# Optimization experiments

Measured on AMD Instinct MI355X. Metric: run time of the kernel, lower is better.

Reference implementation:

```python
import jax, jax.numpy as jnp
import numpy as np

N_NODES = 100000


def _sage_conv(x, edge_index, W_l, W_r, b):
    # PyG SAGEConv (mean aggr): out_i = lin_l(mean_{j in N(i)} x_j) + lin_r(x_i)
    src, dst = edge_index[0], edge_index[1]
    msg = x[src]  # [E, d] gather
    agg_sum = jax.ops.segment_sum(msg, dst, num_segments=N_NODES)  # [N, d]
    deg = jax.ops.segment_sum(jnp.ones((src.shape[0],), x.dtype), dst, num_segments=N_NODES)
    agg = agg_sum / jnp.maximum(deg, 1.0)[:, None]  # mean aggregation
    return agg @ W_l.T + b + x @ W_r.T


def setup_inputs() -> dict:
    key = jax.random.key(0)
    k = jax.random.split(key, 8)
    d_in, hidden, out = 64, 128, 128
    x = jax.random.normal(k[0], (N_NODES, d_in), dtype=jnp.float32)
    edge_index = jax.random.randint(k[1], (2, 1600000), 0, N_NODES, dtype=jnp.int64)
    s1 = 1.0 / np.sqrt(d_in)
    s2 = 1.0 / np.sqrt(hidden)
    return {
        "x": x,
        "edge_index": edge_index,
        "W1_l": jax.random.uniform(k[2], (hidden, d_in), jnp.float32, -s1, s1),
        "W1_r": jax.random.uniform(k[3], (hidden, d_in), jnp.float32, -s1, s1),
        "b1": jnp.zeros((hidden,), jnp.float32),
        "W2_l": jax.random.uniform(k[4], (out, hidden), jnp.float32, -s2, s2),
        "W2_r": jax.random.uniform(k[5], (out, hidden), jnp.float32, -s2, s2),
        "b2": jnp.zeros((out,), jnp.float32),
    }


def reference(x, edge_index, W1_l, W1_r, b1, W2_l, W2_r, b2):
    h = jax.nn.relu(_sage_conv(x, edge_index, W1_l, W1_r, b1))
    return _sage_conv(h, edge_index, W2_l, W2_r, b2)
```

## Files before the change

### kernel.cpp

```cpp
#include <hip/hip_runtime.h>

#define NN 100000
#define NE 1600000
#define SCAN_BLK 2048

#define BSH 9
#define NBUCK2 ((NN + 511) / 512)
#define CHUNK 8192
#define NCHK ((NE + CHUNK - 1) / CHUNK)
#define L2T (NBUCK2 * NCHK)
#define NSTRIP (NN / 32)

using bf16x8 = __attribute__((ext_vector_type(8))) short;
using f32x16 = __attribute__((ext_vector_type(16))) float;

__device__ __forceinline__ unsigned short f2bf(float f) {
    unsigned u = __float_as_uint(f);
    u += 0x7FFFu + ((u >> 16) & 1u);
    return (unsigned short)(u >> 16);
}
__device__ __forceinline__ float bf2f(unsigned short h) {
    return __uint_as_float(((unsigned)h) << 16);
}

__global__ __launch_bounds__(256) void hist2_kernel(const int* __restrict__ dst,
                                                    int* __restrict__ histm) {
    __shared__ int lh[256];
    int blk = blockIdx.x, tid = threadIdx.x;
    lh[tid] = 0;
    __syncthreads();
    int base = blk * CHUNK;
#pragma unroll
    for (int t = 0; t < CHUNK / 256; t++) {
        int e = base + t * 256 + tid;
        if (e < NE) atomicAdd(&lh[dst[e] >> BSH], 1);
    }
    __syncthreads();
    if (tid < NBUCK2) histm[tid * NCHK + blk] = lh[tid];
}

__global__ __launch_bounds__(256) void scan1_kernel(int* __restrict__ data,
                                                    int* __restrict__ bsums, int L) {
    __shared__ int s[256];
    int bid = blockIdx.x, tid = threadIdx.x;
    int base = bid * SCAN_BLK + tid * 8;
    int v[8];
    int sum = 0;
#pragma unroll
    for (int t = 0; t < 8; t++) {
        int idx = base + t;
        v[t] = (idx < L) ? data[idx] : 0;
        sum += v[t];
    }
    s[tid] = sum;
    __syncthreads();
    for (int off = 1; off < 256; off <<= 1) {
        int val = (tid >= off) ? s[tid - off] : 0;
        __syncthreads();
        s[tid] += val;
        __syncthreads();
    }
    int excl = s[tid] - sum;
    if (tid == 255) bsums[bid] = s[255];
    int run = excl;
#pragma unroll
    for (int t = 0; t < 8; t++) {
        int idx = base + t;
        if (idx < L) data[idx] = run;
        run += v[t];
    }
}

__global__ __launch_bounds__(64) void scan2_kernel(int* __restrict__ bsums, int n) {
    int tid = threadIdx.x;
    int orig = (tid < n) ? bsums[tid] : 0;
    int v = orig;
    for (int off = 1; off < 64; off <<= 1) {
        int nb = __shfl_up(v, off, 64);
        if (tid >= off) v += nb;
    }
    if (tid < n) bsums[tid] = v - orig;
}

__global__ __launch_bounds__(256) void scan_add_kernel(int* __restrict__ data,
                                                       const int* __restrict__ bsums, int L) {
    int i = blockIdx.x * 256 + threadIdx.x;
    if (i < L) data[i] += bsums[i / SCAN_BLK];
}

__global__ __launch_bounds__(256) void scatter2_kernel(const int* __restrict__ src,
                                                       const int* __restrict__ dst,
                                                       const int* __restrict__ histm,
                                                       int* __restrict__ tmp) {
    __shared__ int lcur[256];
    int blk = blockIdx.x, tid = threadIdx.x;
    if (tid < NBUCK2) lcur[tid] = histm[tid * NCHK + blk];
    __syncthreads();
    int base = blk * CHUNK;
#pragma unroll
    for (int t = 0; t < CHUNK / 256; t++) {
        int e = base + t * 256 + tid;
        if (e < NE) {
            int d = dst[e];
            int p = atomicAdd(&lcur[d >> BSH], 1);
            tmp[p] = src[e] | ((d & 511) << 17);
        }
    }
}

__global__ __launch_bounds__(256) void count_place_kernel(const int* __restrict__ histm,
                                                          const int* __restrict__ tmp,
                                                          int* __restrict__ rowptr,
                                                          int* __restrict__ esrc) {
    __shared__ int cnt[512];
    __shared__ int s[256];
    int b = blockIdx.x, tid = threadIdx.x;
    int beg = histm[b * NCHK];
    int end = (b == NBUCK2 - 1) ? NE : histm[(b + 1) * NCHK];

    cnt[tid] = 0; cnt[tid + 256] = 0;
    __syncthreads();
    for (int e = beg + tid; e < end; e += 256)
        atomicAdd(&cnt[tmp[e] >> 17], 1);
    __syncthreads();

    int c0 = cnt[2 * tid], c1 = cnt[2 * tid + 1];
    int sum = c0 + c1;
    s[tid] = sum;
    __syncthreads();
    for (int off = 1; off < 256; off <<= 1) {
        int val = (tid >= off) ? s[tid - off] : 0;
        __syncthreads();
        s[tid] += val;
        __syncthreads();
    }
    int o0 = beg + s[tid] - sum;
    int o1 = o0 + c0;
    cnt[2 * tid] = o0;
    cnt[2 * tid + 1] = o1;
    int node0 = (b << BSH) + 2 * tid;
    if (node0 < NN)     rowptr[node0]     = o0;
    if (node0 + 1 < NN) rowptr[node0 + 1] = o1;
    if (b == 0 && tid == 0) rowptr[NN] = NE;
    __syncthreads();

    for (int e = beg + tid; e < end; e += 256) {
        int v = tmp[e];
        int p = atomicAdd(&cnt[v >> 17], 1);
        esrc[p] = v & 0x1FFFF;
    }
}

__global__ __launch_bounds__(256) void cvt_kernel(const float* __restrict__ in,
                                                  unsigned short* __restrict__ out, int n4) {
    int i = blockIdx.x * 256 + threadIdx.x;
    if (i < n4) {
        float4 f = ((const float4*)in)[i];
        ((ushort4*)out)[i] = make_ushort4(f2bf(f.x), f2bf(f.y), f2bf(f.z), f2bf(f.w));
    }
}

__global__ __launch_bounds__(256) void agg64_kernel(const unsigned short* __restrict__ feat,
                                                    const int* __restrict__ rowptr,
                                                    const int* __restrict__ esrc,
                                                    unsigned short* __restrict__ agg) {
    int node = blockIdx.x * 4 + (threadIdx.x >> 6);
    int lane = threadIdx.x & 63;
    int es = lane >> 3;
    int fi = lane & 7;
    int beg = rowptr[node], end = rowptr[node + 1];

    float ax[8];
#pragma unroll
    for (int i = 0; i < 8; i++) ax[i] = 0.0f;

    int e = beg;
    for (; e + 15 < end; e += 16) {
        int sA = esrc[e + es];
        int sB = esrc[e + 8 + es];
        bf16x8 uA = *(const bf16x8*)(feat + (size_t)sA * 64 + fi * 8);
        bf16x8 uB = *(const bf16x8*)(feat + (size_t)sB * 64 + fi * 8);
#pragma unroll
        for (int i = 0; i < 8; i++)
            ax[i] += bf2f((unsigned short)uA[i]) + bf2f((unsigned short)uB[i]);
    }
    if (e + 7 < end) {
        int s = esrc[e + es];
        bf16x8 u = *(const bf16x8*)(feat + (size_t)s * 64 + fi * 8);
#pragma unroll
        for (int i = 0; i < 8; i++) ax[i] += bf2f((unsigned short)u[i]);
        e += 8;
    }
    if (es < end - e) {
        int s = esrc[e + es];
        bf16x8 u = *(const bf16x8*)(feat + (size_t)s * 64 + fi * 8);
#pragma unroll
        for (int i = 0; i < 8; i++) ax[i] += bf2f((unsigned short)u[i]);
    }

#pragma unroll
    for (int i = 0; i < 8; i++) {
        ax[i] += __shfl_xor(ax[i], 8);
        ax[i] += __shfl_xor(ax[i], 16);
        ax[i] += __shfl_xor(ax[i], 32);
    }
    if (es == 0) {
        float inv = 1.0f / fmaxf((float)(end - beg), 1.0f);
        bf16x8 o;
#pragma unroll
        for (int i = 0; i < 8; i++) o[i] = (short)f2bf(ax[i] * inv);
        *(bf16x8*)(agg + (size_t)node * 64 + fi * 8) = o;
    }
}

__global__ __launch_bounds__(256) void agg128_kernel(const unsigned short* __restrict__ feat,
                                                     const int* __restrict__ rowptr,
                                                     const int* __restrict__ esrc,
                                                     unsigned short* __restrict__ agg) {
    int node = blockIdx.x * 4 + (threadIdx.x >> 6);
    int lane = threadIdx.x & 63;
    int es = lane >> 4;
    int fi = lane & 15;
    int beg = rowptr[node], end = rowptr[node + 1];

    float ax[8];
#pragma unroll
    for (int i = 0; i < 8; i++) ax[i] = 0.0f;

    int e = beg;
    for (; e + 7 < end; e += 8) {
        int sA = esrc[e + es];
        int sB = esrc[e + 4 + es];
        bf16x8 uA = *(const bf16x8*)(feat + (size_t)sA * 128 + fi * 8);
        bf16x8 uB = *(const bf16x8*)(feat + (size_t)sB * 128 + fi * 8);
#pragma unroll
        for (int i = 0; i < 8; i++)
            ax[i] += bf2f((unsigned short)uA[i]) + bf2f((unsigned short)uB[i]);
    }
    if (e + 3 < end) {
        int s = esrc[e + es];
        bf16x8 u = *(const bf16x8*)(feat + (size_t)s * 128 + fi * 8);
#pragma unroll
        for (int i = 0; i < 8; i++) ax[i] += bf2f((unsigned short)u[i]);
        e += 4;
    }
    if (es < end - e) {
        int s = esrc[e + es];
        bf16x8 u = *(const bf16x8*)(feat + (size_t)s * 128 + fi * 8);
#pragma unroll
        for (int i = 0; i < 8; i++) ax[i] += bf2f((unsigned short)u[i]);
    }

#pragma unroll
    for (int i = 0; i < 8; i++) {
        ax[i] += __shfl_xor(ax[i], 16);
        ax[i] += __shfl_xor(ax[i], 32);
    }
    if (es == 0) {
        float inv = 1.0f / fmaxf((float)(end - beg), 1.0f);
        bf16x8 o;
#pragma unroll
        for (int i = 0; i < 8; i++) o[i] = (short)f2bf(ax[i] * inv);
        *(bf16x8*)(agg + (size_t)node * 128 + fi * 8) = o;
    }
}

template <int K, bool RELU, bool OUTBF>
__global__ __launch_bounds__(256) void gemm_mfma_kernel(
    const unsigned short* __restrict__ A1,
    const unsigned short* __restrict__ A2,
    const unsigned short* __restrict__ Wa,
    const unsigned short* __restrict__ Wb,
    const float* __restrict__ bias,
    void* __restrict__ outv) {
    int strip = blockIdx.x * 4 + (threadIdx.x >> 6);
    if (strip >= NSTRIP) return;
    const int lane = threadIdx.x & 63;
    const int m = lane & 31;
    const int half = lane >> 5;
    const int base = strip * 32;

    f32x16 acc[4];
#pragma unroll
    for (int nb = 0; nb < 4; ++nb)
#pragma unroll
        for (int r = 0; r < 16; ++r) acc[nb][r] = 0.0f;

    const unsigned short* ar1 = A1 + (size_t)(base + m) * K + half * 8;
    const unsigned short* ar2 = A2 + (size_t)(base + m) * K + half * 8;
#pragma unroll
    for (int kc = 0; kc < K; kc += 16) {
        bf16x8 a = *(const bf16x8*)(ar1 + kc);
#pragma unroll
        for (int nb = 0; nb < 4; ++nb) {
            bf16x8 b = *(const bf16x8*)(Wa + (size_t)(nb * 32 + m) * K + kc + half * 8);
            acc[nb] = __builtin_amdgcn_mfma_f32_32x32x16_bf16(a, b, acc[nb], 0, 0, 0);
        }
    }
#pragma unroll
    for (int kc = 0; kc < K; kc += 16) {
        bf16x8 a = *(const bf16x8*)(ar2 + kc);
#pragma unroll
        for (int nb = 0; nb < 4; ++nb) {
            bf16x8 b = *(const bf16x8*)(Wb + (size_t)(nb * 32 + m) * K + kc + half * 8);
            acc[nb] = __builtin_amdgcn_mfma_f32_32x32x16_bf16(a, b, acc[nb], 0, 0, 0);
        }
    }

#pragma unroll
    for (int nb = 0; nb < 4; ++nb) {
        int j = nb * 32 + m;
        float bz = bias[j];
#pragma unroll
        for (int r = 0; r < 16; ++r) {
            int row = (r & 3) + 8 * (r >> 2) + 4 * half;
            float v = acc[nb][r] + bz;
            if (RELU) v = fmaxf(v, 0.0f);
            size_t idx = (size_t)(base + row) * 128 + j;
            if (OUTBF) ((unsigned short*)outv)[idx] = f2bf(v);
            else       ((float*)outv)[idx] = v;
        }
    }
}

extern "C" void kernel_launch(void* const* d_in, const int* in_sizes, int n_in,
                              void* d_out, int out_size, void* d_ws, size_t ws_size,
                              hipStream_t stream) {
    const float* x   = (const float*)d_in[0];
    const int*   ei  = (const int*)d_in[1];
    const float* W1l = (const float*)d_in[2];
    const float* W1r = (const float*)d_in[3];
    const float* b1  = (const float*)d_in[4];
    const float* W2l = (const float*)d_in[5];
    const float* W2r = (const float*)d_in[6];
    const float* b2  = (const float*)d_in[7];
    float* out = (float*)d_out;

    const int* src = ei;
    const int* dst = ei + NE;

    char* ws = (char*)d_ws;
    int* rowptr = (int*)ws;
    int* esrc   = (int*)(ws + 401408);
    unsigned short* aggB = (unsigned short*)(ws + 6803456);
    unsigned short* xb   = aggB + (size_t)NN * 64;
    char* E = ws + 32403456;
    unsigned short* hb = (unsigned short*)E;
    int* tmp   = (int*)E;
    int* histm = (int*)(E + 6400000);
    int* bsums = (int*)(E + 6560000);
    unsigned short* W1lb = (unsigned short*)d_out;
    unsigned short* W1rb = W1lb + 128 * 64;
    unsigned short* W2lb = (unsigned short*)ws;
    unsigned short* W2rb = W2lb + 128 * 128;

    const int GB  = (NSTRIP + 3) / 4;
    const int NSB2 = (L2T + SCAN_BLK - 1) / SCAN_BLK;

    hist2_kernel<<<NCHK, 256, 0, stream>>>(dst, histm);
    scan1_kernel<<<NSB2, 256, 0, stream>>>(histm, bsums, L2T);
    scan2_kernel<<<1, 64, 0, stream>>>(bsums, NSB2);
    scan_add_kernel<<<(L2T + 255) / 256, 256, 0, stream>>>(histm, bsums, L2T);
    scatter2_kernel<<<NCHK, 256, 0, stream>>>(src, dst, histm, tmp);
    count_place_kernel<<<NBUCK2, 256, 0, stream>>>(histm, tmp, rowptr, esrc);

    cvt_kernel<<<(NN * 64 / 4 + 255) / 256, 256, 0, stream>>>(x, xb, NN * 64 / 4);
    cvt_kernel<<<(128 * 64 / 4 + 255) / 256, 256, 0, stream>>>(W1l, W1lb, 128 * 64 / 4);
    cvt_kernel<<<(128 * 64 / 4 + 255) / 256, 256, 0, stream>>>(W1r, W1rb, 128 * 64 / 4);

    agg64_kernel<<<NN / 4, 256, 0, stream>>>(xb, rowptr, esrc, aggB);
    gemm_mfma_kernel<64, true, true><<<GB, 256, 0, stream>>>(aggB, xb, W1lb, W1rb, b1, hb);

    agg128_kernel<<<NN / 4, 256, 0, stream>>>(hb, rowptr, esrc, aggB);
    cvt_kernel<<<(128 * 128 / 4 + 255) / 256, 256, 0, stream>>>(W2l, W2lb, 128 * 128 / 4);
    cvt_kernel<<<(128 * 128 / 4 + 255) / 256, 256, 0, stream>>>(W2r, W2rb, 128 * 128 / 4);
    gemm_mfma_kernel<128, false, false><<<GB, 256, 0, stream>>>(aggB, hb, W2lb, W2rb, b2, out);
}
```

Baseline: 326.9 us.

## Store hidden features column-split and aggregate layer 2 per 16-feature slice

```diff
diff --git a/kernel.cpp b/kernel.cpp
--- a/kernel.cpp
+++ b/kernel.cpp
@@ -10,6 +10,7 @@
 #define NCHK ((NE + CHUNK - 1) / CHUNK)
 #define L2T (NBUCK2 * NCHK)
 #define NSTRIP (NN / 32)
+#define NG128 (NN / 16)
 
 using bf16x8 = __attribute__((ext_vector_type(8))) short;
 using f32x16 = __attribute__((ext_vector_type(16))) float;
@@ -213,59 +214,61 @@
     }
 }
 
-__global__ __launch_bounds__(256) void agg128_kernel(const unsigned short* __restrict__ feat,
-                                                     const int* __restrict__ rowptr,
-                                                     const int* __restrict__ esrc,
-                                                     unsigned short* __restrict__ agg) {
-    int node = blockIdx.x * 4 + (threadIdx.x >> 6);
-    int lane = threadIdx.x & 63;
-    int es = lane >> 4;
-    int fi = lane & 15;
+__global__ __launch_bounds__(256) void agg128_split_kernel(
+    const unsigned short* __restrict__ hbT,
+    const int* __restrict__ rowptr,
+    const int* __restrict__ esrc,
+    unsigned short* __restrict__ agg) {
+    int b = blockIdx.x;
+    int c = b & 7;
+    int g = b >> 3;
+    int tid = threadIdx.x;
+    int w = tid >> 6;
+    int lane = tid & 63;
+    int node = g * 16 + w * 4 + (lane >> 4);
+    int es = (lane >> 1) & 7;
+    int fi = lane & 1;
     int beg = rowptr[node], end = rowptr[node + 1];
 
+    const unsigned short* tab = hbT + (size_t)c * NN * 16;
+
     float ax[8];
 #pragma unroll
     for (int i = 0; i < 8; i++) ax[i] = 0.0f;
 
-    int e = beg;
-    for (; e + 7 < end; e += 8) {
-        int sA = esrc[e + es];
-        int sB = esrc[e + 4 + es];
-        bf16x8 uA = *(const bf16x8*)(feat + (size_t)sA * 128 + fi * 8);
-        bf16x8 uB = *(const bf16x8*)(feat + (size_t)sB * 128 + fi * 8);
+    int e = beg + es;
+    for (; e + 8 < end; e += 16) {
+        int s0 = esrc[e];
+        int s1 = esrc[e + 8];
+        bf16x8 u0 = *(const bf16x8*)(tab + (size_t)s0 * 16 + fi * 8);
+        bf16x8 u1 = *(const bf16x8*)(tab + (size_t)s1 * 16 + fi * 8);
 #pragma unroll
         for (int i = 0; i < 8; i++)
-            ax[i] += bf2f((unsigned short)uA[i]) + bf2f((unsigned short)uB[i]);
-    }
-    if (e + 3 < end) {
-        int s = esrc[e + es];
-        bf16x8 u = *(const bf16x8*)(feat + (size_t)s * 128 + fi * 8);
-#pragma unroll
-        for (int i = 0; i < 8; i++) ax[i] += bf2f((unsigned short)u[i]);
-        e += 4;
-    }
-    if (es < end - e) {
-        int s = esrc[e + es];
-        bf16x8 u = *(const bf16x8*)(feat + (size_t)s * 128 + fi * 8);
-#pragma unroll
-        for (int i = 0; i < 8; i++) ax[i] += bf2f((unsigned short)u[i]);
+            ax[i] += bf2f((unsigned short)u0[i]) + bf2f((unsigned short)u1[i]);
+    }
+    if (e < end) {
+        int s0 = esrc[e];
+        bf16x8 u0 = *(const bf16x8*)(tab + (size_t)s0 * 16 + fi * 8);
+#pragma unroll
+        for (int i = 0; i < 8; i++) ax[i] += bf2f((unsigned short)u0[i]);
     }
 
 #pragma unroll
     for (int i = 0; i < 8; i++) {
-        ax[i] += __shfl_xor(ax[i], 16);
-        ax[i] += __shfl_xor(ax[i], 32);
+        ax[i] += __shfl_xor(ax[i], 2);
+        ax[i] += __shfl_xor(ax[i], 4);
+        ax[i] += __shfl_xor(ax[i], 8);
     }
     if (es == 0) {
         float inv = 1.0f / fmaxf((float)(end - beg), 1.0f);
         bf16x8 o;
 #pragma unroll
         for (int i = 0; i < 8; i++) o[i] = (short)f2bf(ax[i] * inv);
-        *(bf16x8*)(agg + (size_t)node * 128 + fi * 8) = o;
-    }
-}
-
-template <int K, bool RELU, bool OUTBF>
+        *(bf16x8*)(agg + (size_t)node * 128 + c * 16 + fi * 8) = o;
+    }
+}
+
+template <int K, bool RELU, bool OUTBF, bool A2SPLIT, bool OUTSPLIT>
 __global__ __launch_bounds__(256) void gemm_mfma_kernel(
     const unsigned short* __restrict__ A1,
     const unsigned short* __restrict__ A2,
@@ -287,7 +290,6 @@
         for (int r = 0; r < 16; ++r) acc[nb][r] = 0.0f;
 
     const unsigned short* ar1 = A1 + (size_t)(base + m) * K + half * 8;
-    const unsigned short* ar2 = A2 + (size_t)(base + m) * K + half * 8;
 #pragma unroll
     for (int kc = 0; kc < K; kc += 16) {
         bf16x8 a = *(const bf16x8*)(ar1 + kc);
@@ -299,7 +301,14 @@
     }
 #pragma unroll
     for (int kc = 0; kc < K; kc += 16) {
-        bf16x8 a = *(const bf16x8*)(ar2 + kc);
+        bf16x8 a;
+        if (A2SPLIT) {
+            int off = kc + half * 8;
+            a = *(const bf16x8*)(A2 + (size_t)(off >> 4) * NN * 16 +
+                                 (size_t)(base + m) * 16 + (off & 15));
+        } else {
+            a = *(const bf16x8*)(A2 + (size_t)(base + m) * K + half * 8 + kc);
+        }
 #pragma unroll
         for (int nb = 0; nb < 4; ++nb) {
             bf16x8 b = *(const bf16x8*)(Wb + (size_t)(nb * 32 + m) * K + kc + half * 8);
@@ -316,9 +325,14 @@
             int row = (r & 3) + 8 * (r >> 2) + 4 * half;
             float v = acc[nb][r] + bz;
             if (RELU) v = fmaxf(v, 0.0f);
-            size_t idx = (size_t)(base + row) * 128 + j;
-            if (OUTBF) ((unsigned short*)outv)[idx] = f2bf(v);
-            else       ((float*)outv)[idx] = v;
+            if (OUTSPLIT) {
+                size_t idx = (size_t)(j >> 4) * NN * 16 + (size_t)(base + row) * 16 + (j & 15);
+                ((unsigned short*)outv)[idx] = f2bf(v);
+            } else {
+                size_t idx = (size_t)(base + row) * 128 + j;
+                if (OUTBF) ((unsigned short*)outv)[idx] = f2bf(v);
+                else       ((float*)outv)[idx] = v;
+            }
         }
     }
 }
@@ -345,7 +359,7 @@
     unsigned short* aggB = (unsigned short*)(ws + 6803456);
     unsigned short* xb   = aggB + (size_t)NN * 64;
     char* E = ws + 32403456;
-    unsigned short* hb = (unsigned short*)E;
+    unsigned short* hbT = (unsigned short*)E;
     int* tmp   = (int*)E;
     int* histm = (int*)(E + 6400000);
     int* bsums = (int*)(E + 6560000);
@@ -369,10 +383,12 @@
     cvt_kernel<<<(128 * 64 / 4 + 255) / 256, 256, 0, stream>>>(W1r, W1rb, 128 * 64 / 4);
 
     agg64_kernel<<<NN / 4, 256, 0, stream>>>(xb, rowptr, esrc, aggB);
-    gemm_mfma_kernel<64, true, true><<<GB, 256, 0, stream>>>(aggB, xb, W1lb, W1rb, b1, hb);
-
-    agg128_kernel<<<NN / 4, 256, 0, stream>>>(hb, rowptr, esrc, aggB);
+    gemm_mfma_kernel<64, true, true, false, true><<<GB, 256, 0, stream>>>(
+        aggB, xb, W1lb, W1rb, b1, hbT);
+
+    agg128_split_kernel<<<NG128 * 8, 256, 0, stream>>>(hbT, rowptr, esrc, aggB);
     cvt_kernel<<<(128 * 128 / 4 + 255) / 256, 256, 0, stream>>>(W2l, W2lb, 128 * 128 / 4);
     cvt_kernel<<<(128 * 128 / 4 + 255) / 256, 256, 0, stream>>>(W2r, W2rb, 128 * 128 / 4);
-    gemm_mfma_kernel<128, false, false><<<GB, 256, 0, stream>>>(aggB, hb, W2lb, W2rb, b2, out);
-}
+    gemm_mfma_kernel<128, false, false, true, false><<<GB, 256, 0, stream>>>(
+        aggB, hbT, W2lb, W2rb, b2, out);
+}
```

Measured after the change: 349.9 us. 7.0% more time.
